# Optimization experiments

Hardware: AMD Instinct MI355X
Metric: run time of the kernel (lower is better)

## Reference

```python
import jax, jax.numpy as jnp
import numpy as np

HIDDEN = 256

def setup_inputs() -> dict:
    key = jax.random.key(0)
    k1, k2, k3, k4, k5 = jax.random.split(key, 5)
    hidden = jax.random.normal(k1, (1, 32, HIDDEN), dtype=jnp.float32)
    encoder_outputs = jax.random.normal(k2, (32, 8192, HIDDEN), dtype=jnp.float32)
    # nn.Linear(hidden*2, hidden): weight (H, 2H), bias (H,)
    W = jax.random.normal(k3, (HIDDEN, 2 * HIDDEN), dtype=jnp.float32) / np.sqrt(2 * HIDDEN)
    b = jax.random.normal(k4, (HIDDEN,), dtype=jnp.float32) * 0.01
    v = jax.random.uniform(k5, (HIDDEN,), dtype=jnp.float32)
    return {"hidden": hidden, "encoder_outputs": encoder_outputs, "W": W, "b": b, "v": v}

def reference(hidden, encoder_outputs, W, b, v):
    # hidden: (1, B, H) -> (B, 1, H); avoid materializing the concat by
    # splitting Linear(2H->H) into two matmuls (same math as cat + Linear).
    Wh, We = W[:, :HIDDEN], W[:, HIDDEN:]          # each (H, 2H/2)
    h = jnp.transpose(hidden, (1, 0, 2))           # (B, 1, H)
    # (B,1,H)@(H,H)^T broadcasts over seq; (B,S,H)@(H,H)^T
    pre = jnp.einsum('boh,kh->bok', h, Wh) + jnp.einsum('bsh,kh->bsk', encoder_outputs, We) + b
    scores = jnp.tanh(pre)                          # (B, S, H)
    logits = jnp.einsum('bsh,h->bs', scores, v)     # (B, S)
    attn_weights = jax.nn.softmax(logits, axis=1)   # (B, S)
    context = jnp.einsum('bs,bsh->bh', attn_weights, encoder_outputs)  # (B, H)
    return (context, attn_weights)
```

## Files before the change

### kernel.cpp

```cpp
#include <hip/hip_runtime.h>


typedef _Float16 f16x8 __attribute__((ext_vector_type(8)));
typedef float    f32x4 __attribute__((ext_vector_type(4)));

__device__ __forceinline__ float fast_tanh(float x){
  x = fminf(15.f, fmaxf(-15.f, x));
  float e = __expf(2.f * x);
  return (e - 1.f) * __builtin_amdgcn_rcpf(e + 1.f);
}

__global__ void prep_kernel(const float* __restrict__ hidden, const float* __restrict__ W,
                            const float* __restrict__ bias, _Float16* __restrict__ Bfrag,
                            float* __restrict__ qb)
{
  int blk = blockIdx.x;
  if (blk < 256){
    int tid  = blk * 256 + threadIdx.x;
    int j    = tid & 7;
    int lane = (tid >> 3) & 63;
    int kc   = (tid >> 9) & 7;
    int nt   = tid >> 12;
    int lc   = lane & 15, q = lane >> 4;
    int row  = nt * 16 + lc;
    int col  = 256 + kc * 32 + q * 8 + j;
    Bfrag[tid] = (_Float16)W[row * 512 + col];
  } else {
    int b = blk - 256;
    int k = threadIdx.x;
    const float4* hp = (const float4*)(hidden + b * 256);
    const float4* wp = (const float4*)(W + k * 512);
    float s = 0.f;
    for (int i = 0; i < 64; i++){
      float4 h4 = hp[i], w4 = wp[i];
      s += h4.x * w4.x + h4.y * w4.y + h4.z * w4.z + h4.w * w4.w;
    }
    qb[b * 256 + k] = s + bias[k];
  }
}

__global__ __launch_bounds__(512, 2) void attn_main(
    const float* __restrict__ enc, const _Float16* __restrict__ Bfrag,
    const float* __restrict__ qb, const float* __restrict__ v,
    float* __restrict__ logits, float* __restrict__ P,
    float* __restrict__ mw, float* __restrict__ lw)
{
  __shared__ _Float16 Bs[16384];
  __shared__ float sl[128];
  __shared__ float Pl[256];
  __shared__ float red[16];

  const int b = blockIdx.x >> 6, chunk = blockIdx.x & 63;
  const int tid = threadIdx.x, wv = tid >> 6, lane = tid & 63;
  const int q = lane >> 4, lc = lane & 15;
  const int rowBase = b * 8192 + chunk * 128;
  const int waveRow = wv * 16;

  if (tid < 256) Pl[tid] = 0.f;

  f16x8 A[8];
  {
    const float* rp = enc + (size_t)(rowBase + waveRow + lc) * 256 + q * 8;
    #pragma unroll
    for (int kc = 0; kc < 8; kc++){
      const float4* p = (const float4*)(rp + kc * 32);
      float4 x0 = p[0], x1 = p[1];
      f16x8 af;
      af[0] = (_Float16)x0.x; af[1] = (_Float16)x0.y; af[2] = (_Float16)x0.z; af[3] = (_Float16)x0.w;
      af[4] = (_Float16)x1.x; af[5] = (_Float16)x1.y; af[6] = (_Float16)x1.z; af[7] = (_Float16)x1.w;
      A[kc] = af;
    }
  }

  float plog[4] = {0, 0, 0, 0};
  const float* qbB = qb + b * 256;

  for (int h = 0; h < 4; h++){
    __syncthreads();
    {
      const f16x8* src = (const f16x8*)(Bfrag + h * 16384);
      f16x8* dst = (f16x8*)Bs;
      #pragma unroll
      for (int i = 0; i < 4; i++) dst[tid + i * 512] = src[tid + i * 512];
    }
    __syncthreads();
    #pragma unroll
    for (int ntl = 0; ntl < 4; ntl++){
      const int nt = h * 4 + ntl;
      f32x4 acc = {0, 0, 0, 0};
      const f16x8* bp = ((const f16x8*)Bs) + ntl * 512 + lane;
      #pragma unroll
      for (int kc = 0; kc < 8; kc++){
        f16x8 bf = bp[kc * 64];
        acc = __builtin_amdgcn_mfma_f32_16x16x32_f16(A[kc], bf, acc, 0, 0, 0);
      }
      const int col = nt * 16 + lc;
      const float qv = qbB[col], vv = v[col];
      #pragma unroll
      for (int r = 0; r < 4; r++)
        plog[r] += fast_tanh(acc[r] + qv) * vv;
    }
  }

  #pragma unroll
  for (int r = 0; r < 4; r++){
    float s = plog[r];
    s += __shfl_xor(s, 1); s += __shfl_xor(s, 2);
    s += __shfl_xor(s, 4); s += __shfl_xor(s, 8);
    plog[r] = s;
  }
  if (lc == 0){
    #pragma unroll
    for (int r = 0; r < 4; r++){
      int rl = waveRow + q * 4 + r;
      sl[rl] = plog[r];
      logits[rowBase + rl] = plog[r];
    }
  }
  __syncthreads();

  if (tid < 128){
    float x = sl[tid], m = x;
    for (int o = 1; o < 64; o <<= 1) m = fmaxf(m, __shfl_xor(m, o));
    if (lane == 0) red[wv] = m;
  }
  __syncthreads();
  if (tid == 0) red[8] = fmaxf(red[0], red[1]);
  __syncthreads();
  const float M = red[8];
  if (tid < 128){
    float e = __expf(sl[tid] - M);
    sl[tid] = e;
    float s2 = e;
    for (int o = 1; o < 64; o <<= 1) s2 += __shfl_xor(s2, o);
    if (lane == 0) red[wv] = s2;
  }
  __syncthreads();
  if (tid == 0){ mw[blockIdx.x] = M; lw[blockIdx.x] = red[0] + red[1]; }

  const float w0 = sl[waveRow + lc];
  #pragma unroll
  for (int kc = 0; kc < 8; kc++){
    float c8[8];
    #pragma unroll
    for (int j = 0; j < 8; j++)
      c8[j] = w0 * (float)A[kc][j];
    #pragma unroll
    for (int j = 0; j < 8; j++){
      float s = c8[j];
      s += __shfl_xor(s, 1); s += __shfl_xor(s, 2);
      s += __shfl_xor(s, 4); s += __shfl_xor(s, 8);
      c8[j] = s;
    }
    if (lc == 0){
      #pragma unroll
      for (int j = 0; j < 8; j++) atomicAdd(&Pl[kc * 32 + q * 8 + j], c8[j]);
    }
  }
  __syncthreads();
  if (tid < 256) P[(size_t)blockIdx.x * 256 + tid] = Pl[tid];
}

__global__ void attn_finish(const float* __restrict__ logits, const float* __restrict__ P,
                            const float* __restrict__ mw, const float* __restrict__ lw,
                            float* __restrict__ out)
{
  const int b = blockIdx.x, t = threadIdx.x;
  __shared__ float sm[64], sw[64];
  if (t < 64){ sm[t] = mw[b * 64 + t]; sw[t] = lw[b * 64 + t]; }
  __syncthreads();
  float M = -1e30f;
  for (int i = 0; i < 64; i++) M = fmaxf(M, sm[i]);
  float L = 0.f;
  for (int i = 0; i < 64; i++) L += sw[i] * __expf(sm[i] - M);
  const float inv = 1.f / L;
  float c = 0.f;
  for (int ch = 0; ch < 64; ch++) c += __expf(sm[ch] - M) * P[(size_t)(b * 64 + ch) * 256 + t];
  out[b * 256 + t] = c * inv;
  const float* lg = logits + (size_t)b * 8192;
  float* ao = out + 8192 + (size_t)b * 8192;
  for (int s = t; s < 8192; s += 256) ao[s] = __expf(lg[s] - M) * inv;
}

extern "C" void kernel_launch(void* const* d_in, const int* in_sizes, int n_in,
                              void* d_out, int out_size, void* d_ws, size_t ws_size,
                              hipStream_t stream)
{
  const float* hidden = (const float*)d_in[0];
  const float* enc    = (const float*)d_in[1];
  const float* W      = (const float*)d_in[2];
  const float* bias   = (const float*)d_in[3];
  const float* v      = (const float*)d_in[4];
  float* out = (float*)d_out;

  char* ws = (char*)d_ws;
  _Float16* Bfrag = (_Float16*)ws;
  float* qb     = (float*)(ws + (128 << 10));
  float* logits = (float*)(ws + (160 << 10));
  float* P      = (float*)(ws + (160 << 10) + (1 << 20));
  float* mw     = (float*)(ws + (160 << 10) + (3 << 20));
  float* lw     = (float*)(ws + (160 << 10) + (3 << 20) + (8 << 10));

  prep_kernel<<<288, 256, 0, stream>>>(hidden, W, bias, Bfrag, qb);
  attn_main<<<2048, 512, 0, stream>>>(enc, Bfrag, qb, v, logits, P, mw, lw);
  attn_finish<<<32, 256, 0, stream>>>(logits, P, mw, lw, out);
}
```

Measured before the change: 505.7 us.

## Halve attention block size to 64 rows and 256 threads, doubling grid

```diff
diff --git a/kernel.cpp b/kernel.cpp
--- a/kernel.cpp
+++ b/kernel.cpp
@@ -39,24 +39,23 @@
   }
 }
 
-__global__ __launch_bounds__(512, 2) void attn_main(
+__global__ __launch_bounds__(256) void attn_main(
     const float* __restrict__ enc, const _Float16* __restrict__ Bfrag,
     const float* __restrict__ qb, const float* __restrict__ v,
     float* __restrict__ logits, float* __restrict__ P,
     float* __restrict__ mw, float* __restrict__ lw)
 {
-  __shared__ _Float16 Bs[16384];
-  __shared__ float sl[128];
+  __shared__ _Float16 Bs[8192];
+  __shared__ float sl[64];
   __shared__ float Pl[256];
-  __shared__ float red[16];
-
-  const int b = blockIdx.x >> 6, chunk = blockIdx.x & 63;
+
+  const int b = blockIdx.x >> 7, chunk = blockIdx.x & 127;
   const int tid = threadIdx.x, wv = tid >> 6, lane = tid & 63;
   const int q = lane >> 4, lc = lane & 15;
-  const int rowBase = b * 8192 + chunk * 128;
+  const int rowBase = b * 8192 + chunk * 64;
   const int waveRow = wv * 16;
 
-  if (tid < 256) Pl[tid] = 0.f;
+  Pl[tid] = 0.f;
 
   f16x8 A[8];
   {
@@ -75,18 +74,18 @@
   float plog[4] = {0, 0, 0, 0};
   const float* qbB = qb + b * 256;
 
-  for (int h = 0; h < 4; h++){
+  for (int h = 0; h < 8; h++){
     __syncthreads();
     {
-      const f16x8* src = (const f16x8*)(Bfrag + h * 16384);
+      const f16x8* src = (const f16x8*)(Bfrag + h * 8192);
       f16x8* dst = (f16x8*)Bs;
       #pragma unroll
-      for (int i = 0; i < 4; i++) dst[tid + i * 512] = src[tid + i * 512];
+      for (int i = 0; i < 4; i++) dst[tid + i * 256] = src[tid + i * 256];
     }
     __syncthreads();
     #pragma unroll
-    for (int ntl = 0; ntl < 4; ntl++){
-      const int nt = h * 4 + ntl;
+    for (int ntl = 0; ntl < 2; ntl++){
+      const int nt = h * 2 + ntl;
       f32x4 acc = {0, 0, 0, 0};
       const f16x8* bp = ((const f16x8*)Bs) + ntl * 512 + lane;
       #pragma unroll
@@ -119,24 +118,17 @@
   }
   __syncthreads();
 
-  if (tid < 128){
-    float x = sl[tid], m = x;
+  if (tid < 64){
+    float x = sl[tid];
+    float m = x;
     for (int o = 1; o < 64; o <<= 1) m = fmaxf(m, __shfl_xor(m, o));
-    if (lane == 0) red[wv] = m;
-  }
-  __syncthreads();
-  if (tid == 0) red[8] = fmaxf(red[0], red[1]);
-  __syncthreads();
-  const float M = red[8];
-  if (tid < 128){
-    float e = __expf(sl[tid] - M);
+    float e = __expf(x - m);
     sl[tid] = e;
     float s2 = e;
     for (int o = 1; o < 64; o <<= 1) s2 += __shfl_xor(s2, o);
-    if (lane == 0) red[wv] = s2;
-  }
-  __syncthreads();
-  if (tid == 0){ mw[blockIdx.x] = M; lw[blockIdx.x] = red[0] + red[1]; }
+    if (tid == 0){ mw[blockIdx.x] = m; lw[blockIdx.x] = s2; }
+  }
+  __syncthreads();
 
   const float w0 = sl[waveRow + lc];
   #pragma unroll
@@ -158,7 +150,7 @@
     }
   }
   __syncthreads();
-  if (tid < 256) P[(size_t)blockIdx.x * 256 + tid] = Pl[tid];
+  P[(size_t)blockIdx.x * 256 + tid] = Pl[tid];
 }
 
 __global__ void attn_finish(const float* __restrict__ logits, const float* __restrict__ P,
@@ -166,16 +158,27 @@
                             float* __restrict__ out)
 {
   const int b = blockIdx.x, t = threadIdx.x;
-  __shared__ float sm[64], sw[64];
-  if (t < 64){ sm[t] = mw[b * 64 + t]; sw[t] = lw[b * 64 + t]; }
-  __syncthreads();
-  float M = -1e30f;
-  for (int i = 0; i < 64; i++) M = fmaxf(M, sm[i]);
-  float L = 0.f;
-  for (int i = 0; i < 64; i++) L += sw[i] * __expf(sm[i] - M);
-  const float inv = 1.f / L;
+  __shared__ float sm[128], sw[128], se[128], sM[1], sL[1];
+  if (t < 128){ sm[t] = mw[b * 128 + t]; sw[t] = lw[b * 128 + t]; }
+  __syncthreads();
+  if (t == 0){
+    float M = -1e30f;
+    for (int i = 0; i < 128; i++) M = fmaxf(M, sm[i]);
+    sM[0] = M;
+  }
+  __syncthreads();
+  const float M = sM[0];
+  if (t < 128) se[t] = __expf(sm[t] - M);
+  __syncthreads();
+  if (t == 0){
+    float L = 0.f;
+    for (int i = 0; i < 128; i++) L += sw[i] * se[i];
+    sL[0] = L;
+  }
+  __syncthreads();
+  const float inv = 1.f / sL[0];
   float c = 0.f;
-  for (int ch = 0; ch < 64; ch++) c += __expf(sm[ch] - M) * P[(size_t)(b * 64 + ch) * 256 + t];
+  for (int ch = 0; ch < 128; ch++) c += se[ch] * P[(size_t)(b * 128 + ch) * 256 + t];
   out[b * 256 + t] = c * inv;
   const float* lg = logits + (size_t)b * 8192;
   float* ao = out + 8192 + (size_t)b * 8192;
@@ -198,10 +201,10 @@
   float* qb     = (float*)(ws + (128 << 10));
   float* logits = (float*)(ws + (160 << 10));
   float* P      = (float*)(ws + (160 << 10) + (1 << 20));
-  float* mw     = (float*)(ws + (160 << 10) + (3 << 20));
-  float* lw     = (float*)(ws + (160 << 10) + (3 << 20) + (8 << 10));
+  float* mw     = (float*)(ws + (160 << 10) + (5 << 20));
+  float* lw     = (float*)(ws + (160 << 10) + (5 << 20) + (16 << 10));
 
   prep_kernel<<<288, 256, 0, stream>>>(hidden, W, bias, Bfrag, qb);
-  attn_main<<<2048, 512, 0, stream>>>(enc, Bfrag, qb, v, logits, P, mw, lw);
+  attn_main<<<4096, 256, 0, stream>>>(enc, Bfrag, qb, v, logits, P, mw, lw);
   attn_finish<<<32, 256, 0, stream>>>(logits, P, mw, lw, out);
 }
```

New measurement: 459.6 us. 9.1% less time.
